# Optimization experiments

Hardware: AMD Instinct MI355X
Metric: run time of the kernel (lower is better)

The kernel has to match this reference:

```python
import jax, jax.numpy as jnp
import numpy as np
import math


def _neighbor_stack(x):
    # x: [b, nc, w, d] -> [b, nc, 3, w, d] with zero-padded prev/next chunks
    prev = jnp.pad(x[:, :-1], ((0, 0), (1, 0), (0, 0), (0, 0)))
    nxt = jnp.pad(x[:, 1:], ((0, 0), (0, 1), (0, 0), (0, 0)))
    return jnp.stack([prev, x, nxt], axis=2)


def local_attention(q, kv, Wq, Wkv, Wo, w):
    b, L, d_model = q.shape
    d_head = Wkv.shape[1] // 2
    h = d_model // d_head
    nc = L // w

    qp = (q @ Wq).reshape(b, L, h, d_head) / math.sqrt(d_head)
    kvp = kv @ Wkv  # [b, L, 2*d_head], single shared KV head (MQA)
    k, v = kvp[..., :d_head], kvp[..., d_head:]

    cq = qp.reshape(b, nc, w, h, d_head)
    k3 = _neighbor_stack(k.reshape(b, nc, w, d_head))  # [b, nc, 3, w, d]
    v3 = _neighbor_stack(v.reshape(b, nc, w, d_head))  # [b, nc, 3, w, d]

    # scores over (prev, self, next) chunks; padded edge chunks contribute
    # zero scores (exp(0)=1 in softmax), exactly as the torch F.pad(value=0) does.
    scores = jnp.einsum('bcxhd,bcpyd->bcxhpy', cq, k3)  # [b,nc,w,h,3,w]
    probs = jax.nn.softmax(scores.reshape(b, nc, w, h, 3 * w), axis=-1)
    probs = probs.reshape(b, nc, w, h, 3, w)

    ctx = jnp.einsum('bcxhpy,bcpyd->bcxhd', probs, v3)  # [b,nc,w,h,d]
    ctx = ctx.reshape(b, L, d_model)
    return ctx @ Wo


def setup_inputs() -> dict:
    key = jax.random.key(0)
    k1, k2, k3, k4, k5 = jax.random.split(key, 5)
    b, L, d_model, n_head = 1, 4096, 1024, 16
    d_head = d_model // n_head
    scale = 0.02
    return {
        'q': jax.random.normal(k1, (b, L, d_model), dtype=jnp.float32),
        'kv': jax.random.normal(k2, (b, L, d_model), dtype=jnp.float32),
        'Wq': jax.random.normal(k3, (d_model, d_model), dtype=jnp.float32) * scale,
        'Wkv': jax.random.normal(k4, (d_model, 2 * d_head), dtype=jnp.float32) * scale,
        'Wo': jax.random.normal(k5, (d_model, d_model), dtype=jnp.float32) * scale,
        'w': 512,
    }


def reference(q, kv, Wq, Wkv, Wo, w):
    return local_attention(q, kv, Wq, Wkv, Wo, w)
```

## Files before the change

### kernel.cpp

```cpp
#include <hip/hip_runtime.h>
#include <hip/hip_bf16.h>

typedef unsigned short u16;
typedef unsigned int u32;
typedef __attribute__((ext_vector_type(8))) short bf16x8;
typedef __attribute__((ext_vector_type(4))) float f32x4;
typedef __attribute__((ext_vector_type(16))) float f32x16;
typedef __attribute__((ext_vector_type(4))) u32 u32x4;

__device__ __forceinline__ u16 f2bf(float x) {
  __hip_bfloat16 h = __float2bfloat16(x);
  return __builtin_bit_cast(u16, h);
}

__device__ __forceinline__ u32 pkbf(float lo, float hi) {
  return (u32)f2bf(lo) | ((u32)f2bf(hi) << 16);
}

__device__ __forceinline__ bf16x8 mk_frag(u32 a, u32 b, u32 c, u32 d) {
  u32x4 v = {a, b, c, d};
  return __builtin_bit_cast(bf16x8, v);
}

__device__ __forceinline__ f32x16 mfma32(bf16x8 a, bf16x8 b, f32x16 c) {
  return __builtin_amdgcn_mfma_f32_32x32x16_bf16(a, b, c, 0, 0, 0);
}

__device__ __forceinline__ void gload16(const void* g, void* lds) {
  __builtin_amdgcn_global_load_lds((const __attribute__((address_space(1))) void*)g,
                                   (__attribute__((address_space(3))) void*)lds, 16, 0, 0);
}

__global__ __launch_bounds__(256) void cvt_tw(const float* __restrict__ q, const float* __restrict__ kv,
                                              const float* __restrict__ Wq, const float* __restrict__ Wkv,
                                              const float* __restrict__ Wo, u16* __restrict__ qkbf,
                                              u16* __restrict__ wqt, u16* __restrict__ wkvt,
                                              u16* __restrict__ wot) {
  __shared__ float T[64][65];
  const int t = threadIdx.x;
  const int bid = blockIdx.x;
  if (bid < 4096) {
    int idx = bid * 256 + t;
    const float* src = (idx < 524288) ? q : kv;
    int li = idx & 524287;
    const float4* p = (const float4*)src + (size_t)li * 2;
    float4 a = p[0], b = p[1];
    bf16x8 vv;
    vv[0] = (short)f2bf(a.x); vv[1] = (short)f2bf(a.y);
    vv[2] = (short)f2bf(a.z); vv[3] = (short)f2bf(a.w);
    vv[4] = (short)f2bf(b.x); vv[5] = (short)f2bf(b.y);
    vv[6] = (short)f2bf(b.z); vv[7] = (short)f2bf(b.w);
    *(bf16x8*)(qkbf + (size_t)idx * 8) = vv;
    return;
  }
  const int wb = bid - 4096;
  const float* W; u16* Wt; int N, bx, by;
  if (wb < 256)      { W = Wq;  Wt = wqt;  N = 1024; bx = wb & 15; by = wb >> 4; }
  else if (wb < 512) { int b = wb - 256; W = Wo;  Wt = wot;  N = 1024; bx = b & 15; by = b >> 4; }
  else               { int b = wb - 512; W = Wkv; Wt = wkvt; N = 128;  bx = b & 1;  by = b >> 1; }
  const int K = 1024;
  const int n0 = bx * 64, k0 = by * 64;
  #pragma unroll
  for (int pass = 0; pass < 4; ++pass) {
    int r = pass * 16 + (t >> 4);
    int c = (t & 15) * 4;
    float4 v = *(const float4*)(W + (size_t)(k0 + r) * N + n0 + c);
    T[r][c] = v.x; T[r][c + 1] = v.y; T[r][c + 2] = v.z; T[r][c + 3] = v.w;
  }
  __syncthreads();
  #pragma unroll
  for (int s = 0; s < 2; ++s) {
    int n = s * 32 + (t >> 3);
    int kk = (t & 7) * 8;
    bf16x8 vv;
    #pragma unroll
    for (int i = 0; i < 8; ++i) vv[i] = (short)f2bf(T[kk + i][n]);
    *(bf16x8*)(Wt + (size_t)(n0 + n) * K + k0 + kk) = vv;
  }
}

template<int BF16OUT>
__global__ __launch_bounds__(256, 2) void gemm_bt(const u16* __restrict__ A, const u16* __restrict__ Bt,
                                                  void* __restrict__ Cout, int N, int K, float scale) {
  __shared__ __attribute__((aligned(16))) u16 As[128 * 64];
  __shared__ __attribute__((aligned(16))) u16 Bs[64 * 64];
  const int t = threadIdx.x;
  const int lane = t & 63, wv = t >> 6;
  const int g = lane >> 4, i16 = lane & 15;
  const int m0 = blockIdx.y * 128, n0 = blockIdx.x * 64;
  const int wr = wv >> 1, wc = wv & 1;
  f32x4 acc[4][2] = {};
  for (int kt = 0; kt < K; kt += 64) {
    #pragma unroll
    for (int j = 0; j < 4; ++j) {
      int p = j * 4096 + t * 16;
      int row = p >> 7;
      int lg = (p & 127) ^ ((row & 7) << 4);
      gload16(A + (size_t)(m0 + row) * K + kt + (lg >> 1), (char*)As + j * 4096 + wv * 1024);
    }
    #pragma unroll
    for (int j = 0; j < 2; ++j) {
      int p = j * 4096 + t * 16;
      int row = p >> 7;
      int lg = (p & 127) ^ ((row & 7) << 4);
      gload16(Bt + (size_t)(n0 + row) * K + kt + (lg >> 1), (char*)Bs + j * 4096 + wv * 1024);
    }
    __syncthreads();
    bf16x8 af[2][4], bfr[2][2];
    #pragma unroll
    for (int kf = 0; kf < 2; ++kf) {
      #pragma unroll
      for (int x = 0; x < 4; ++x) {
        int ra = wr * 64 + x * 16 + i16;
        af[kf][x] = *(const bf16x8*)((const char*)As + ((ra * 128 + kf * 64 + g * 16) ^ ((ra & 7) << 4)));
      }
      #pragma unroll
      for (int x = 0; x < 2; ++x) {
        int rb = wc * 32 + x * 16 + i16;
        bfr[kf][x] = *(const bf16x8*)((const char*)Bs + ((rb * 128 + kf * 64 + g * 16) ^ ((rb & 7) << 4)));
      }
    }
    #pragma unroll
    for (int kf = 0; kf < 2; ++kf)
      #pragma unroll
      for (int mi = 0; mi < 4; ++mi)
        #pragma unroll
        for (int ni = 0; ni < 2; ++ni)
          acc[mi][ni] = __builtin_amdgcn_mfma_f32_16x16x32_bf16(af[kf][mi], bfr[kf][ni], acc[mi][ni], 0, 0, 0);
    __syncthreads();
  }
  #pragma unroll
  for (int mi = 0; mi < 4; ++mi)
    #pragma unroll
    for (int ni = 0; ni < 2; ++ni)
      #pragma unroll
      for (int r = 0; r < 4; ++r) {
        size_t off = (size_t)(m0 + wr * 64 + mi * 16 + g * 4 + r) * N + (n0 + wc * 32 + ni * 16 + i16);
        float v = acc[mi][ni][r] * scale;
        if (BF16OUT) ((u16*)Cout)[off] = f2bf(v);
        else ((float*)Cout)[off] = v;
      }
}

__global__ __launch_bounds__(256, 2) void gemm_qkv(const u16* __restrict__ qbf, const u16* __restrict__ kvbf,
                                                   const u16* __restrict__ wqt, const u16* __restrict__ wkvt,
                                                   u16* __restrict__ qp, u16* __restrict__ kvp,
                                                   u16* __restrict__ vtg) {
  __shared__ __attribute__((aligned(16))) u16 As[128 * 64];
  __shared__ __attribute__((aligned(16))) u16 Bs[64 * 64];
  const int t = threadIdx.x;
  const int lane = t & 63, wv = t >> 6;
  const int g = lane >> 4, i16 = lane & 15;
  const int wr = wv >> 1, wc = wv & 1;
  const int K = 1024;
  const int bid = blockIdx.x;
  const bool iskv = bid >= 512;
  const u16* A; const u16* Bt; int m0, n0;
  if (!iskv) { A = qbf;  Bt = wqt;  m0 = (bid >> 4) * 128; n0 = (bid & 15) * 64; }
  else       { int b = bid - 512; A = kvbf; Bt = wkvt; m0 = (b >> 1) * 128; n0 = (b & 1) * 64; }
  f32x4 acc[4][2] = {};
  for (int kt = 0; kt < K; kt += 64) {
    #pragma unroll
    for (int j = 0; j < 4; ++j) {
      int p = j * 4096 + t * 16;
      int row = p >> 7;
      int lg = (p & 127) ^ ((row & 7) << 4);
      gload16(A + (size_t)(m0 + row) * K + kt + (lg >> 1), (char*)As + j * 4096 + wv * 1024);
    }
    #pragma unroll
    for (int j = 0; j < 2; ++j) {
      int p = j * 4096 + t * 16;
      int row = p >> 7;
      int lg = (p & 127) ^ ((row & 7) << 4);
      gload16(Bt + (size_t)(n0 + row) * K + kt + (lg >> 1), (char*)Bs + j * 4096 + wv * 1024);
    }
    __syncthreads();
    bf16x8 af[2][4], bfr[2][2];
    #pragma unroll
    for (int kf = 0; kf < 2; ++kf) {
      #pragma unroll
      for (int x = 0; x < 4; ++x) {
        int ra = wr * 64 + x * 16 + i16;
        af[kf][x] = *(const bf16x8*)((const char*)As + ((ra * 128 + kf * 64 + g * 16) ^ ((ra & 7) << 4)));
      }
      #pragma unroll
      for (int x = 0; x < 2; ++x) {
        int rb = wc * 32 + x * 16 + i16;
        bfr[kf][x] = *(const bf16x8*)((const char*)Bs + ((rb * 128 + kf * 64 + g * 16) ^ ((rb & 7) << 4)));
      }
    }
    #pragma unroll
    for (int kf = 0; kf < 2; ++kf)
      #pragma unroll
      for (int mi = 0; mi < 4; ++mi)
        #pragma unroll
        for (int ni = 0; ni < 2; ++ni)
          acc[mi][ni] = __builtin_amdgcn_mfma_f32_16x16x32_bf16(af[kf][mi], bfr[kf][ni], acc[mi][ni], 0, 0, 0);
    __syncthreads();
  }
  if (!iskv) {
    #pragma unroll
    for (int mi = 0; mi < 4; ++mi)
      #pragma unroll
      for (int ni = 0; ni < 2; ++ni)
        #pragma unroll
        for (int r = 0; r < 4; ++r)
          qp[(size_t)(m0 + wr * 64 + mi * 16 + g * 4 + r) * 1024 + n0 + wc * 32 + ni * 16 + i16] =
              f2bf(acc[mi][ni][r] * 0.125f);
  } else if (n0 == 0) {
    #pragma unroll
    for (int mi = 0; mi < 4; ++mi)
      #pragma unroll
      for (int ni = 0; ni < 2; ++ni)
        #pragma unroll
        for (int r = 0; r < 4; ++r)
          kvp[(size_t)(m0 + wr * 64 + mi * 16 + g * 4 + r) * 64 + wc * 32 + ni * 16 + i16] =
              f2bf(acc[mi][ni][r]);
  } else {
    u16* CT = (u16*)As;
    #pragma unroll
    for (int mi = 0; mi < 4; ++mi)
      #pragma unroll
      for (int ni = 0; ni < 2; ++ni)
        #pragma unroll
        for (int r = 0; r < 4; ++r)
          CT[(wc * 32 + ni * 16 + i16) * 128 + wr * 64 + mi * 16 + g * 4 + r] = f2bf(acc[mi][ni][r]);
    __syncthreads();
    int d = t >> 2, c4 = t & 3;
    const u16* src = CT + d * 128 + c4 * 32;
    u16* dst = vtg + (size_t)d * 4096 + m0 + c4 * 32;
    #pragma unroll
    for (int j = 0; j < 4; ++j)
      *(bf16x8*)(dst + j * 8) = *(const bf16x8*)(src + j * 8);
  }
}

__global__ __launch_bounds__(256, 2) void attn_kernel(const u16* __restrict__ qp, const u16* __restrict__ kvp,
                                                      const u16* __restrict__ vtg, u16* __restrict__ ctx) {
  __shared__ __attribute__((aligned(16))) u16 Ks[3][64 * 64];
  __shared__ __attribute__((aligned(16))) u16 Vs[3][64 * 64];
  const int t = threadIdx.x;
  const int lane = t & 63, wv = t >> 6;
  const int hh = lane >> 5, q32 = lane & 31;
  const int bid = blockIdx.x;
  const int qt = bid & 3, hd = (bid >> 2) & 15, c = bid >> 6;
  const int q0 = c * 512 + qt * 128 + wv * 32;
  const int pk32 = (q32 & 19) | ((q32 & 4) << 1) | ((q32 & 8) >> 1);

  bf16x8 qf[4];
  #pragma unroll
  for (int dt = 0; dt < 4; ++dt)
    qf[dt] = *(const bf16x8*)(qp + (size_t)(q0 + q32) * 1024 + hd * 64 + dt * 16 + hh * 8);

  const int kb0 = (c - 1) * 512;
  const int v0 = (c == 0) ? 8 : 0;
  const int v1 = (c == 7) ? 15 : 23;
  const int nv = v1 - v0 + 1;
  float l = 32.f * (float)(24 - nv);
  f32x16 accO[2] = {};

  int kA[2], vA[2];
  #pragma unroll
  for (int j = 0; j < 2; ++j) {
    int p = j * 4096 + t * 16;
    int row = p >> 7;
    int lg = (p & 127) ^ ((row & 7) << 4);
    kA[j] = row * 64 + (lg >> 1);
    vA[j] = row * 4096 + (lg >> 1);
  }

  auto stage = [&](int b, int kb) {
    #pragma unroll
    for (int j = 0; j < 2; ++j)
      gload16(kvp + (size_t)(kb * 64 + kA[j]), (char*)Ks[b] + j * 4096 + t * 16);
    #pragma unroll
    for (int j = 0; j < 2; ++j)
      gload16(vtg + (size_t)(kb + vA[j]), (char*)Vs[b] + j * 4096 + t * 16);
  };

  stage(0, kb0 + v0 * 64);
  stage(1, kb0 + (v0 + 1) * 64);

  for (int i = 0; i < nv; ++i) {
    if (i + 1 < nv) asm volatile("s_waitcnt vmcnt(4)" ::: "memory");
    else            asm volatile("s_waitcnt vmcnt(0)" ::: "memory");
    __builtin_amdgcn_s_barrier();
    if (i + 2 < nv) stage((i + 2) % 3, kb0 + (v0 + i + 2) * 64);
    const int buf = i % 3;
    const char* kbase0 = (const char*)Ks[buf];
    const char* vbase0 = (const char*)Vs[buf];
    f32x16 s[2] = {};
    #pragma unroll
    for (int kt = 0; kt < 2; ++kt) {
      const char* kbase = kbase0 + kt * 4096 + pk32 * 128;
      int kswz = (pk32 & 7) << 4;
      #pragma unroll
      for (int dt = 0; dt < 4; ++dt) {
        bf16x8 kf = *(const bf16x8*)(kbase + ((dt * 32 + hh * 16) ^ kswz));
        s[kt] = mfma32(kf, qf[dt], s[kt]);
      }
    }
    #pragma unroll
    for (int kt = 0; kt < 2; ++kt) {
      float pv[16];
      #pragma unroll
      for (int r = 0; r < 16; ++r) pv[r] = __expf(s[kt][r]);
      l += (((pv[0] + pv[1]) + (pv[2] + pv[3])) + ((pv[4] + pv[5]) + (pv[6] + pv[7]))) +
           (((pv[8] + pv[9]) + (pv[10] + pv[11])) + ((pv[12] + pv[13]) + (pv[14] + pv[15])));
      u32 w[8];
      #pragma unroll
      for (int j = 0; j < 8; ++j) w[j] = pkbf(pv[2 * j], pv[2 * j + 1]);
      bf16x8 pb0 = mk_frag(w[0], w[1], w[2], w[3]);
      bf16x8 pb1 = mk_frag(w[4], w[5], w[6], w[7]);
      int vswz = (q32 & 7) << 4;
      #pragma unroll
      for (int dtv = 0; dtv < 2; ++dtv) {
        const char* vbase = vbase0 + dtv * 4096 + q32 * 128;
        bf16x8 va0 = *(const bf16x8*)(vbase + ((kt * 64 + hh * 16) ^ vswz));
        accO[dtv] = mfma32(va0, pb0, accO[dtv]);
        bf16x8 va1 = *(const bf16x8*)(vbase + ((kt * 64 + 32 + hh * 16) ^ vswz));
        accO[dtv] = mfma32(va1, pb1, accO[dtv]);
      }
    }
  }
  l += __shfl_xor(l, 32);
  float rl = 1.0f / l;
  __syncthreads();
  char* Ow = (char*)Ks[0] + wv * 4096;
  #pragma unroll
  for (int dtv = 0; dtv < 2; ++dtv)
    #pragma unroll
    for (int j = 0; j < 4; ++j) {
      int d = dtv * 32 + 8 * j + 4 * hh;
      uint2 wp;
      wp.x = pkbf(accO[dtv][4 * j] * rl, accO[dtv][4 * j + 1] * rl);
      wp.y = pkbf(accO[dtv][4 * j + 2] * rl, accO[dtv][4 * j + 3] * rl);
      *(uint2*)(Ow + q32 * 128 + ((d * 2) ^ ((q32 & 7) << 4))) = wp;
    }
  asm volatile("s_waitcnt lgkmcnt(0)" ::: "memory");
  __builtin_amdgcn_sched_barrier(0);
  #pragma unroll
  for (int rep = 0; rep < 4; ++rep) {
    int q = lane >> 1, dblk = (lane & 1) * 4 + rep, d0 = dblk * 8;
    bf16x8 ov = *(const bf16x8*)(Ow + q * 128 + ((d0 * 2) ^ ((q & 7) << 4)));
    *(bf16x8*)(ctx + (size_t)(q0 + q) * 1024 + hd * 64 + d0) = ov;
  }
}

extern "C" void kernel_launch(void* const* d_in, const int* in_sizes, int n_in,
                              void* d_out, int out_size, void* d_ws, size_t ws_size,
                              hipStream_t stream) {
  const float* q   = (const float*)d_in[0];
  const float* kv  = (const float*)d_in[1];
  const float* Wq  = (const float*)d_in[2];
  const float* Wkv = (const float*)d_in[3];
  const float* Wo  = (const float*)d_in[4];
  char* ws = (char*)d_ws;
  u16* qbf  = (u16*)(ws);
  u16* ctx  = (u16*)(ws);
  u16* kvbf = (u16*)(ws + 8388608);
  u16* qp   = (u16*)(ws + 16777216);
  u16* kvp  = (u16*)(ws + 25165824);
  u16* vtg  = (u16*)(ws + 25690112);
  u16* wqt  = (u16*)(ws + 26214400);
  u16* wkvt = (u16*)(ws + 28311552);
  u16* wot  = (u16*)(ws + 28573696);
  cvt_tw<<<4640, 256, 0, stream>>>(q, kv, Wq, Wkv, Wo, qbf, wqt, wkvt, wot);
  gemm_qkv<<<576, 256, 0, stream>>>(qbf, kvbf, wqt, wkvt, qp, kvp, vtg);
  attn_kernel<<<512, 256, 0, stream>>>(qp, kvp, vtg, ctx);
  gemm_bt<0><<<dim3(16, 32), 256, 0, stream>>>(ctx, wot, (float*)d_out, 1024, 1024, 1.0f);
}
```

Baseline: 91.96 us.

## Split attention key range across two wave groups and merge partial results in LDS

Doubles the attention block to 512 threads. The two groups of four waves each process half of the key/value tiles for the same queries, each group with its own double-buffered LDS staging. The second group writes its partial output and row sums to LDS, and the first group adds them, normalises, and stores. The goal is more waves in flight per query tile to hide latency on a small grid. The cost is an extra LDS reduction and barrier, and a pipeline that drops from three buffers to two and waits for all loads each step.

```diff
diff --git a/kernel.cpp b/kernel.cpp
--- a/kernel.cpp
+++ b/kernel.cpp
@@ -235,16 +235,18 @@
   }
 }
 
-__global__ __launch_bounds__(256, 2) void attn_kernel(const u16* __restrict__ qp, const u16* __restrict__ kvp,
+__global__ __launch_bounds__(512, 4) void attn_kernel(const u16* __restrict__ qp, const u16* __restrict__ kvp,
                                                       const u16* __restrict__ vtg, u16* __restrict__ ctx) {
-  __shared__ __attribute__((aligned(16))) u16 Ks[3][64 * 64];
-  __shared__ __attribute__((aligned(16))) u16 Vs[3][64 * 64];
+  __shared__ __attribute__((aligned(16))) u16 Ks[2][2][64 * 64];
+  __shared__ __attribute__((aligned(16))) u16 Vs[2][2][64 * 64];
   const int t = threadIdx.x;
   const int lane = t & 63, wv = t >> 6;
+  const int g2 = wv >> 2, wq = wv & 3;
+  const int tg = t & 255;
   const int hh = lane >> 5, q32 = lane & 31;
   const int bid = blockIdx.x;
   const int qt = bid & 3, hd = (bid >> 2) & 15, c = bid >> 6;
-  const int q0 = c * 512 + qt * 128 + wv * 32;
+  const int q0 = c * 512 + qt * 128 + wq * 32;
   const int pk32 = (q32 & 19) | ((q32 & 4) << 1) | ((q32 & 8) >> 1);
 
   bf16x8 qf[4];
@@ -254,41 +256,40 @@
 
   const int kb0 = (c - 1) * 512;
   const int v0 = (c == 0) ? 8 : 0;
-  const int v1 = (c == 7) ? 15 : 23;
-  const int nv = v1 - v0 + 1;
-  float l = 32.f * (float)(24 - nv);
+  const int nv = (c == 0 || c == 7) ? 16 : 24;
+  const int n2 = nv >> 1;
+  const int s0 = v0 + g2 * n2;
+  float l = g2 ? 0.f : 32.f * (float)(24 - nv);
   f32x16 accO[2] = {};
 
   int kA[2], vA[2];
   #pragma unroll
   for (int j = 0; j < 2; ++j) {
-    int p = j * 4096 + t * 16;
+    int p = j * 4096 + tg * 16;
     int row = p >> 7;
     int lg = (p & 127) ^ ((row & 7) << 4);
     kA[j] = row * 64 + (lg >> 1);
     vA[j] = row * 4096 + (lg >> 1);
   }
 
-  auto stage = [&](int b, int kb) {
+  auto stage = [&](int b, int tile) {
+    const int kb = kb0 + tile * 64;
     #pragma unroll
     for (int j = 0; j < 2; ++j)
-      gload16(kvp + (size_t)(kb * 64 + kA[j]), (char*)Ks[b] + j * 4096 + t * 16);
+      gload16(kvp + (size_t)(kb * 64 + kA[j]), (char*)Ks[g2][b] + j * 4096 + tg * 16);
     #pragma unroll
     for (int j = 0; j < 2; ++j)
-      gload16(vtg + (size_t)(kb + vA[j]), (char*)Vs[b] + j * 4096 + t * 16);
+      gload16(vtg + (size_t)(kb + vA[j]), (char*)Vs[g2][b] + j * 4096 + tg * 16);
   };
 
-  stage(0, kb0 + v0 * 64);
-  stage(1, kb0 + (v0 + 1) * 64);
-
-  for (int i = 0; i < nv; ++i) {
-    if (i + 1 < nv) asm volatile("s_waitcnt vmcnt(4)" ::: "memory");
-    else            asm volatile("s_waitcnt vmcnt(0)" ::: "memory");
+  stage(0, s0);
+
+  for (int i = 0; i < n2; ++i) {
+    asm volatile("s_waitcnt vmcnt(0)" ::: "memory");
     __builtin_amdgcn_s_barrier();
-    if (i + 2 < nv) stage((i + 2) % 3, kb0 + (v0 + i + 2) * 64);
-    const int buf = i % 3;
-    const char* kbase0 = (const char*)Ks[buf];
-    const char* vbase0 = (const char*)Vs[buf];
+    if (i + 1 < n2) stage((i + 1) & 1, s0 + i + 1);
+    const char* kbase0 = (const char*)Ks[g2][i & 1];
+    const char* vbase0 = (const char*)Vs[g2][i & 1];
     f32x16 s[2] = {};
     #pragma unroll
     for (int kt = 0; kt < 2; ++kt) {
@@ -302,14 +303,13 @@
     }
     #pragma unroll
     for (int kt = 0; kt < 2; ++kt) {
-      float pv[16];
-      #pragma unroll
-      for (int r = 0; r < 16; ++r) pv[r] = __expf(s[kt][r]);
-      l += (((pv[0] + pv[1]) + (pv[2] + pv[3])) + ((pv[4] + pv[5]) + (pv[6] + pv[7]))) +
-           (((pv[8] + pv[9]) + (pv[10] + pv[11])) + ((pv[12] + pv[13]) + (pv[14] + pv[15])));
+      #pragma unroll
+      for (int r = 0; r < 16; ++r) s[kt][r] = __expf(s[kt][r]);
+      l += (((s[kt][0] + s[kt][1]) + (s[kt][2] + s[kt][3])) + ((s[kt][4] + s[kt][5]) + (s[kt][6] + s[kt][7]))) +
+           (((s[kt][8] + s[kt][9]) + (s[kt][10] + s[kt][11])) + ((s[kt][12] + s[kt][13]) + (s[kt][14] + s[kt][15])));
       u32 w[8];
       #pragma unroll
-      for (int j = 0; j < 8; ++j) w[j] = pkbf(pv[2 * j], pv[2 * j + 1]);
+      for (int j = 0; j < 8; ++j) w[j] = pkbf(s[kt][2 * j], s[kt][2 * j + 1]);
       bf16x8 pb0 = mk_frag(w[0], w[1], w[2], w[3]);
       bf16x8 pb1 = mk_frag(w[4], w[5], w[6], w[7]);
       int vswz = (q32 & 7) << 4;
@@ -323,27 +323,54 @@
       }
     }
   }
-  l += __shfl_xor(l, 32);
-  float rl = 1.0f / l;
+
   __syncthreads();
-  char* Ow = (char*)Ks[0] + wv * 4096;
-  #pragma unroll
-  for (int dtv = 0; dtv < 2; ++dtv)
-    #pragma unroll
-    for (int j = 0; j < 4; ++j) {
-      int d = dtv * 32 + 8 * j + 4 * hh;
-      uint2 wp;
-      wp.x = pkbf(accO[dtv][4 * j] * rl, accO[dtv][4 * j + 1] * rl);
-      wp.y = pkbf(accO[dtv][4 * j + 2] * rl, accO[dtv][4 * j + 3] * rl);
-      *(uint2*)(Ow + q32 * 128 + ((d * 2) ^ ((q32 & 7) << 4))) = wp;
-    }
-  asm volatile("s_waitcnt lgkmcnt(0)" ::: "memory");
-  __builtin_amdgcn_sched_barrier(0);
-  #pragma unroll
-  for (int rep = 0; rep < 4; ++rep) {
-    int q = lane >> 1, dblk = (lane & 1) * 4 + rep, d0 = dblk * 8;
-    bf16x8 ov = *(const bf16x8*)(Ow + q * 128 + ((d0 * 2) ^ ((q & 7) << 4)));
-    *(bf16x8*)(ctx + (size_t)(q0 + q) * 1024 + hd * 64 + d0) = ov;
+  char* M = (char*)&Ks[0][0][0];
+  float* Lx = (float*)&Vs[0][0][0];
+  if (g2 == 1) {
+    #pragma unroll
+    for (int dtv = 0; dtv < 2; ++dtv)
+      #pragma unroll
+      for (int j = 0; j < 4; ++j) {
+        f32x4 chunk = {accO[dtv][4 * j], accO[dtv][4 * j + 1], accO[dtv][4 * j + 2], accO[dtv][4 * j + 3]};
+        int byte = lane * 128 + dtv * 64 + j * 16;
+        *(f32x4*)(M + wq * 8192 + (byte ^ ((lane & 7) << 4))) = chunk;
+      }
+    Lx[wq * 64 + lane] = l;
+  }
+  __syncthreads();
+  if (g2 == 0) {
+    #pragma unroll
+    for (int dtv = 0; dtv < 2; ++dtv)
+      #pragma unroll
+      for (int j = 0; j < 4; ++j) {
+        int byte = lane * 128 + dtv * 64 + j * 16;
+        f32x4 chunk = *(const f32x4*)(M + wq * 8192 + (byte ^ ((lane & 7) << 4)));
+        #pragma unroll
+        for (int e = 0; e < 4; ++e) accO[dtv][4 * j + e] += chunk[e];
+      }
+    l += Lx[wq * 64 + lane];
+    l += __shfl_xor(l, 32);
+    float rl = 1.0f / l;
+    char* Ow = (char*)&Vs[1][0][0] + wq * 4096;
+    #pragma unroll
+    for (int dtv = 0; dtv < 2; ++dtv)
+      #pragma unroll
+      for (int j = 0; j < 4; ++j) {
+        int d = dtv * 32 + 8 * j + 4 * hh;
+        uint2 wp;
+        wp.x = pkbf(accO[dtv][4 * j] * rl, accO[dtv][4 * j + 1] * rl);
+        wp.y = pkbf(accO[dtv][4 * j + 2] * rl, accO[dtv][4 * j + 3] * rl);
+        *(uint2*)(Ow + q32 * 128 + ((d * 2) ^ ((q32 & 7) << 4))) = wp;
+      }
+    asm volatile("s_waitcnt lgkmcnt(0)" ::: "memory");
+    __builtin_amdgcn_sched_barrier(0);
+    #pragma unroll
+    for (int rep = 0; rep < 4; ++rep) {
+      int q = lane >> 1, dblk = (lane & 1) * 4 + rep, d0 = dblk * 8;
+      bf16x8 ov = *(const bf16x8*)(Ow + q * 128 + ((d0 * 2) ^ ((q & 7) << 4)));
+      *(bf16x8*)(ctx + (size_t)(q0 - wq * 32 + wq * 32 + q) * 1024 + hd * 64 + d0) = ov;
+    }
   }
 }
 
@@ -367,6 +394,6 @@
   u16* wot  = (u16*)(ws + 28573696);
   cvt_tw<<<4640, 256, 0, stream>>>(q, kv, Wq, Wkv, Wo, qbf, wqt, wkvt, wot);
   gemm_qkv<<<576, 256, 0, stream>>>(qbf, kvbf, wqt, wkvt, qp, kvp, vtg);
-  attn_kernel<<<512, 256, 0, stream>>>(qp, kvp, vtg, ctx);
+  attn_kernel<<<512, 512, 0, stream>>>(qp, kvp, vtg, ctx);
   gemm_bt<0><<<dim3(16, 32), 256, 0, stream>>>(ctx, wot, (float*)d_out, 1024, 1024, 1.0f);
 }
```

New measurement: 92.62 us. About the same (+0.7%).
